# Kernel optimization log

Hardware: AMD Instinct MI355X
Metric: run time of the kernel (lower is better)

The kernel has to match this reference:

```python
import jax, jax.numpy as jnp
import numpy as np

N_NODES = 100000
N_EDGES = 3200000
N_GRAPHS = 256
D = 3
H = 32


def _pointnet_layer(h, pos, src, dst, Wa, ba, Wb, bb):
    # PyG convention: edge_index = [src(j), dst(i)]; message uses h_j, pos_j - pos_i
    edge_feat = jnp.concatenate([h[src], pos[src] - pos[dst]], axis=-1)  # [E, Cin+D]
    msg = jax.nn.relu(edge_feat @ Wa + ba) @ Wb + bb                     # [E, H]
    agg = jax.ops.segment_max(msg, dst, num_segments=N_NODES)           # [N, H]
    # PyG scatter-max fills nodes with no incoming edges with 0
    return jnp.where(jnp.isneginf(agg), 0.0, agg)


def setup_inputs() -> dict:
    key = jax.random.key(0)
    ks = jax.random.split(key, 12)
    pos = jax.random.normal(ks[0], (N_NODES, D), dtype=jnp.float32)
    edge_index = jax.random.randint(ks[1], (2, N_EDGES), 0, N_NODES, dtype=jnp.int32)
    batch = jnp.sort(jax.random.randint(ks[2], (N_NODES,), 0, N_GRAPHS, dtype=jnp.int32))
    def lin(k, fan_in, fan_out):
        bound = 1.0 / np.sqrt(fan_in)
        kw, kb = jax.random.split(k)
        W = jax.random.uniform(kw, (fan_in, fan_out), minval=-bound, maxval=bound, dtype=jnp.float32)
        b = jax.random.uniform(kb, (fan_out,), minval=-bound, maxval=bound, dtype=jnp.float32)
        return W, b
    W1a, b1a = lin(ks[3], D + D, H)
    W1b, b1b = lin(ks[4], H, H)
    W2a, b2a = lin(ks[5], H + D, H)
    W2b, b2b = lin(ks[6], H, H)
    Wout, bout = lin(ks[7], H, 1)
    return {"pos": pos, "edge_index": edge_index, "batch": batch,
            "W1a": W1a, "b1a": b1a, "W1b": W1b, "b1b": b1b,
            "W2a": W2a, "b2a": b2a, "W2b": W2b, "b2b": b2b,
            "Wout": Wout, "bout": bout}


def reference(pos, edge_index, batch, W1a, b1a, W1b, b1b, W2a, b2a, W2b, b2b, Wout, bout):
    src, dst = edge_index[0], edge_index[1]
    h = _pointnet_layer(pos, pos, src, dst, W1a, b1a, W1b, b1b)
    h = jax.nn.relu(h)
    h = _pointnet_layer(h, pos, src, dst, W2a, b2a, W2b, b2b)
    h = jax.nn.relu(h)
    g = jax.ops.segment_max(h, batch, num_segments=N_GRAPHS)  # global_max_pool -> [B, H]
    g = jnp.where(jnp.isneginf(g), 0.0, g)
    return g @ Wout + bout  # [B, 1]
```

## Files before the change

### kernel.cpp

```cpp
#include <hip/hip_runtime.h>

#define NN 100000
#define NE 3200000
#define NG 256
#define H 32
#define SB ((NN + 255) / 256)

typedef __attribute__((ext_vector_type(8))) short b16x8;
typedef __attribute__((ext_vector_type(4))) float f32x4;

union ABfrag { unsigned u[4]; b16x8 v; };

__global__ __launch_bounds__(256) void k_init(unsigned* __restrict__ g,
                                              unsigned* __restrict__ hist) {
    int i = blockIdx.x * 256 + threadIdx.x;
    if (i < NG * H) g[i] = 0u;
    if (i < NN) hist[i] = 0u;
}

__global__ __launch_bounds__(64) void k_packw(const float* __restrict__ W1b,
                                              const float* __restrict__ W2b,
                                              unsigned* __restrict__ Wpk) {
    int l = threadIdx.x;
    int n = l & 15, gq = l >> 4;
    for (int layer = 0; layer < 2; layer++) {
        const float* W = layer ? W2b : W1b;
        for (int h = 0; h < 2; h++) {
            unsigned hi[8], lo[8];
#pragma unroll
            for (int i = 0; i < 8; i++) {
                float w = W[(8 * gq + i) * H + h * 16 + n];
                unsigned wb = __float_as_uint(w);
                unsigned hb = wb & 0xffff0000u;
                float r = w - __uint_as_float(hb);
                hi[i] = hb;
                lo[i] = __float_as_uint(r) & 0xffff0000u;
            }
            unsigned* dh = Wpk + (((layer * 4 + h * 2 + 0) * 64) + l) * 4;
            unsigned* dl = Wpk + (((layer * 4 + h * 2 + 1) * 64) + l) * 4;
#pragma unroll
            for (int w2 = 0; w2 < 4; w2++) {
                dh[w2] = (hi[2 * w2] >> 16) | (hi[2 * w2 + 1] & 0xffff0000u);
                dl[w2] = (lo[2 * w2] >> 16) | (lo[2 * w2 + 1] & 0xffff0000u);
            }
        }
    }
}

__global__ __launch_bounds__(256) void k_hist(const int* __restrict__ dst,
                                              unsigned* __restrict__ hist) {
    int e = blockIdx.x * 256 + threadIdx.x;
    atomicAdd(&hist[dst[e]], 1u);
}

__global__ __launch_bounds__(256) void k_scan1(const unsigned* __restrict__ hist,
                                               unsigned* __restrict__ pre,
                                               unsigned* __restrict__ bsum) {
    __shared__ unsigned sd[256];
    int tid = threadIdx.x;
    int i = blockIdx.x * 256 + tid;
    unsigned v = (i < NN) ? hist[i] : 0u;
    sd[tid] = v;
    __syncthreads();
    for (int off = 1; off < 256; off <<= 1) {
        unsigned t = (tid >= off) ? sd[tid - off] : 0u;
        __syncthreads();
        sd[tid] += t;
        __syncthreads();
    }
    if (i < NN) pre[i] = sd[tid] - v;
    if (tid == 255) bsum[blockIdx.x] = sd[255];
}

__global__ __launch_bounds__(512) void k_scan2(const unsigned* __restrict__ bsum,
                                               unsigned* __restrict__ bpre) {
    __shared__ unsigned sd[512];
    int t = threadIdx.x;
    unsigned v = (t < SB) ? bsum[t] : 0u;
    sd[t] = v;
    __syncthreads();
    for (int off = 1; off < 512; off <<= 1) {
        unsigned x = (t >= off) ? sd[t - off] : 0u;
        __syncthreads();
        sd[t] += x;
        __syncthreads();
    }
    if (t < SB) bpre[t] = sd[t] - v;
}

__global__ __launch_bounds__(256) void k_scan3(const unsigned* __restrict__ pre,
                                               const unsigned* __restrict__ bpre,
                                               const unsigned* __restrict__ hist,
                                               unsigned* __restrict__ cursors,
                                               unsigned* __restrict__ ends) {
    int i = blockIdx.x * 256 + threadIdx.x;
    if (i < NN) {
        unsigned o = pre[i] + bpre[blockIdx.x];
        cursors[i] = o;
        ends[i] = o + hist[i];
    }
}

__global__ __launch_bounds__(256) void k_scatter(const int* __restrict__ src,
                                                 const int* __restrict__ dst,
                                                 unsigned* __restrict__ cursors,
                                                 unsigned* __restrict__ srcS) {
    int e = blockIdx.x * 256 + threadIdx.x;
    int d = dst[e];
    unsigned slot = atomicAdd(&cursors[d], 1u);
    srcS[slot] = (unsigned)src[e];
}

__global__ __launch_bounds__(256) void k_pre1(const float* __restrict__ pos,
                                              const float* __restrict__ W1a,
                                              const float* __restrict__ b1a,
                                              float* __restrict__ E) {
    int n = blockIdx.x * 256 + threadIdx.x;
    if (n >= NN) return;
    float p0 = pos[3 * n], p1 = pos[3 * n + 1], p2 = pos[3 * n + 2];
    float ev[H];
#pragma unroll
    for (int k = 0; k < H; k++) {
        float v = b1a[k];
        v = fmaf(p0, W1a[k] + W1a[96 + k], v);
        v = fmaf(p1, W1a[32 + k] + W1a[128 + k], v);
        v = fmaf(p2, W1a[64 + k] + W1a[160 + k], v);
        ev[k] = v;
    }
    float4* E4 = (float4*)(E + (size_t)n * H);
#pragma unroll
    for (int r = 0; r < 8; r++)
        E4[r] = make_float4(ev[4 * r], ev[4 * r + 1], ev[4 * r + 2], ev[4 * r + 3]);
}

__global__ __launch_bounds__(256) void k_pre2(const float* __restrict__ pos,
                                              const float* __restrict__ agg,
                                              const float* __restrict__ W2a,
                                              const float* __restrict__ b2a,
                                              float* __restrict__ E) {
    int n = blockIdx.x * 256 + threadIdx.x;
    if (n >= NN) return;
    float h[H];
    const float4* A4 = (const float4*)(agg + (size_t)n * H);
#pragma unroll
    for (int r = 0; r < 8; r++) {
        float4 u = A4[r];
        h[4 * r + 0] = u.x; h[4 * r + 1] = u.y;
        h[4 * r + 2] = u.z; h[4 * r + 3] = u.w;
    }
    float p0 = pos[3 * n], p1 = pos[3 * n + 1], p2 = pos[3 * n + 2];
    float ev[H];
#pragma unroll
    for (int k = 0; k < H; k++) {
        float v = b2a[k];
        v = fmaf(p0, W2a[32 * H + k], v);
        v = fmaf(p1, W2a[33 * H + k], v);
        v = fmaf(p2, W2a[34 * H + k], v);
        ev[k] = v;
    }
#pragma unroll
    for (int j = 0; j < H; j++) {
        float hj = h[j];
#pragma unroll
        for (int k = 0; k < H; k++) ev[k] = fmaf(hj, W2a[j * H + k], ev[k]);
    }
    float4* E4 = (float4*)(E + (size_t)n * H);
#pragma unroll
    for (int r = 0; r < 8; r++)
        E4[r] = make_float4(ev[4 * r], ev[4 * r + 1], ev[4 * r + 2], ev[4 * r + 3]);
}

__global__ __launch_bounds__(256) void k_edge(const unsigned* __restrict__ srcS,
                                              const unsigned* __restrict__ ends,
                                              const float* __restrict__ pos,
                                              const float* __restrict__ E,
                                              const float* __restrict__ Wf,
                                              const unsigned* __restrict__ WpkL,
                                              const float* __restrict__ bb,
                                              float* __restrict__ aggOut,
                                              const int* __restrict__ batch,
                                              unsigned* __restrict__ g,
                                              int layer2) {
    int lane = threadIdx.x & 63;
    int node = __builtin_amdgcn_readfirstlane(blockIdx.x * 4 + (threadIdx.x >> 6));
    unsigned start = (node == 0) ? 0u : ends[node - 1];
    int deg = (int)(ends[node] - start);
    int row = lane & 15;
    int j0 = (lane >> 4) << 3;
    ABfrag b0h, b0l, b1h, b1l;
    {
        const uint4* W4 = (const uint4*)WpkL;
        *(uint4*)b0h.u = W4[0 * 64 + lane];
        *(uint4*)b0l.u = W4[1 * 64 + lane];
        *(uint4*)b1h.u = W4[2 * 64 + lane];
        *(uint4*)b1l.u = W4[3 * 64 + lane];
    }
    float pd0 = pos[3 * node], pd1 = pos[3 * node + 1], pd2 = pos[3 * node + 2];
    float fd[8];
#pragma unroll
    for (int q = 0; q < 8; q++)
        fd[q] = fmaf(pd0, Wf[j0 + q],
                fmaf(pd1, Wf[32 + j0 + q], pd2 * Wf[64 + j0 + q]));
    f32x4 vmax0 = {-3.0e38f, -3.0e38f, -3.0e38f, -3.0e38f};
    f32x4 vmax1 = vmax0;
    const f32x4 z = {0.f, 0.f, 0.f, 0.f};
    for (int i0 = 0; i0 < deg; i0 += 16) {
        int e = i0 + row;
        if (e >= deg) e = deg - 1;
        int s = (int)srcS[start + e];
        const float* er = E + ((size_t)s << 5) + j0;
        float4 t0 = *(const float4*)er;
        float4 t1 = *(const float4*)(er + 4);
        float t[8] = {t0.x, t0.y, t0.z, t0.w, t1.x, t1.y, t1.z, t1.w};
        ABfrag ah, al;
#pragma unroll
        for (int w = 0; w < 4; w++) {
            float x0 = fmaxf(t[2 * w]     - fd[2 * w],     0.f);
            float x1 = fmaxf(t[2 * w + 1] - fd[2 * w + 1], 0.f);
            unsigned u0 = __float_as_uint(x0), u1 = __float_as_uint(x1);
            ah.u[w] = __builtin_amdgcn_perm(u1, u0, 0x07060302u);
            float r0 = x0 - __uint_as_float(u0 & 0xffff0000u);
            float r1 = x1 - __uint_as_float(u1 & 0xffff0000u);
            al.u[w] = __builtin_amdgcn_perm(__float_as_uint(r1),
                                            __float_as_uint(r0), 0x07060302u);
        }
        f32x4 acc0 = __builtin_amdgcn_mfma_f32_16x16x32_bf16(ah.v, b0h.v, z, 0, 0, 0);
        acc0 = __builtin_amdgcn_mfma_f32_16x16x32_bf16(al.v, b0h.v, acc0, 0, 0, 0);
        acc0 = __builtin_amdgcn_mfma_f32_16x16x32_bf16(ah.v, b0l.v, acc0, 0, 0, 0);
        f32x4 acc1 = __builtin_amdgcn_mfma_f32_16x16x32_bf16(ah.v, b1h.v, z, 0, 0, 0);
        acc1 = __builtin_amdgcn_mfma_f32_16x16x32_bf16(al.v, b1h.v, acc1, 0, 0, 0);
        acc1 = __builtin_amdgcn_mfma_f32_16x16x32_bf16(ah.v, b1l.v, acc1, 0, 0, 0);
#pragma unroll
        for (int r = 0; r < 4; r++) {
            vmax0[r] = fmaxf(vmax0[r], acc0[r]);
            vmax1[r] = fmaxf(vmax1[r], acc1[r]);
        }
    }
    float m0 = fmaxf(fmaxf(vmax0[0], vmax0[1]), fmaxf(vmax0[2], vmax0[3]));
    float m1 = fmaxf(fmaxf(vmax1[0], vmax1[1]), fmaxf(vmax1[2], vmax1[3]));
    m0 = fmaxf(m0, __shfl_xor(m0, 16));
    m0 = fmaxf(m0, __shfl_xor(m0, 32));
    m1 = fmaxf(m1, __shfl_xor(m1, 16));
    m1 = fmaxf(m1, __shfl_xor(m1, 32));
    if (lane < H) {
        float red = (lane < 16) ? m0 : m1;
        float val = (deg > 0) ? fmaxf(red + bb[lane], 0.f) : 0.f;
        if (!layer2) {
            aggOut[(size_t)node * H + lane] = val;
        } else {
            int b = batch[node];
            unsigned bits = __float_as_uint(val);
            unsigned* gb = g + ((size_t)b << 5) + lane;
            if (bits > *gb) atomicMax(gb, bits);
        }
    }
}

__global__ __launch_bounds__(256) void k_out(const unsigned* __restrict__ g,
                                             const float* __restrict__ Wout,
                                             const float* __restrict__ bout,
                                             float* __restrict__ out) {
    int bidx = threadIdx.x;
    float acc = bout[0];
#pragma unroll
    for (int k = 0; k < H; k++)
        acc = fmaf(__uint_as_float(g[bidx * H + k]), Wout[k], acc);
    out[bidx] = acc;
}

extern "C" void kernel_launch(void* const* d_in, const int* in_sizes, int n_in,
                              void* d_out, int out_size, void* d_ws, size_t ws_size,
                              hipStream_t stream) {
    const float* pos  = (const float*)d_in[0];
    const int* src    = (const int*)d_in[1];
    const int* dst    = src + NE;
    const int* batch  = (const int*)d_in[2];
    const float* W1a  = (const float*)d_in[3];
    const float* b1a  = (const float*)d_in[4];
    const float* W1b  = (const float*)d_in[5];
    const float* b1b  = (const float*)d_in[6];
    const float* W2a  = (const float*)d_in[7];
    const float* b2a  = (const float*)d_in[8];
    const float* W2b  = (const float*)d_in[9];
    const float* b2b  = (const float*)d_in[10];
    const float* Wout = (const float*)d_in[11];
    const float* bout = (const float*)d_in[12];
    float* out = (float*)d_out;

    const size_t SZ = (size_t)NN * H;
    float*    agg  = (float*)d_ws;
    float*    E    = (float*)d_ws + SZ;
    unsigned* srcS = (unsigned*)d_ws + 2 * SZ;
    unsigned* g    = (unsigned*)d_ws + 3 * SZ;
    unsigned* ends = g + NG * H;
    unsigned* bsum = ends + NN;
    unsigned* bpre = bsum + SB + 1;
    unsigned* Wpk  = bpre + SB + 1;
    unsigned* hist    = (unsigned*)agg;
    unsigned* pre     = hist + NN;
    unsigned* cursors = pre + NN;

    const int EDGE_BLOCKS = NE / 256;
    const int NODE_BLOCKS = SB;
    const int WAVE_BLOCKS = NN / 4;

    k_init<<<NODE_BLOCKS, 256, 0, stream>>>(g, hist);
    k_packw<<<1, 64, 0, stream>>>(W1b, W2b, Wpk);
    k_hist<<<EDGE_BLOCKS, 256, 0, stream>>>(dst, hist);
    k_scan1<<<NODE_BLOCKS, 256, 0, stream>>>(hist, pre, bsum);
    k_scan2<<<1, 512, 0, stream>>>(bsum, bpre);
    k_scan3<<<NODE_BLOCKS, 256, 0, stream>>>(pre, bpre, hist, cursors, ends);
    k_scatter<<<EDGE_BLOCKS, 256, 0, stream>>>(src, dst, cursors, srcS);
    k_pre1<<<NODE_BLOCKS, 256, 0, stream>>>(pos, W1a, b1a, E);
    k_edge<<<WAVE_BLOCKS, 256, 0, stream>>>(srcS, ends, pos, E,
                                            W1a + 3 * H, Wpk, b1b,
                                            agg, batch, g, 0);
    k_pre2<<<NODE_BLOCKS, 256, 0, stream>>>(pos, agg, W2a, b2a, E);
    k_edge<<<WAVE_BLOCKS, 256, 0, stream>>>(srcS, ends, pos, E,
                                            W2a + 32 * H, Wpk + 1024, b2b,
                                            agg, batch, g, 1);
    k_out<<<1, 256, 0, stream>>>(g, Wout, bout, out);
}
```

Measured before the change: 758.3 us.

## Two-pass bucketed CSR scatter to localize atomic and write traffic

Replaces the single random scatter of edges into CSR order with a two-pass approach. The first pass partitions edges into 98 coarse destination buckets of 1024 nodes each, using block-local histograms and a packed src/dst-low-bits staging buffer. The second pass does the per-node atomic cursor scatter with bucket-local addresses, which should improve cache locality of atomics and srcS writes. The cost is an extra pass over all edges, a binary search per edge, and reuse of the E buffer as staging.

```diff
diff --git a/kernel.cpp b/kernel.cpp
--- a/kernel.cpp
+++ b/kernel.cpp
@@ -5,6 +5,9 @@
 #define NG 256
 #define H 32
 #define SB ((NN + 255) / 256)
+#define NB 98
+#define BK_SH 10
+#define PART_BLOCKS ((NE + 4095) / 4096)
 
 typedef __attribute__((ext_vector_type(8))) short b16x8;
 typedef __attribute__((ext_vector_type(4))) float f32x4;
@@ -12,10 +15,12 @@
 union ABfrag { unsigned u[4]; b16x8 v; };
 
 __global__ __launch_bounds__(256) void k_init(unsigned* __restrict__ g,
-                                              unsigned* __restrict__ hist) {
+                                              unsigned* __restrict__ hist,
+                                              unsigned* __restrict__ bktcnt) {
     int i = blockIdx.x * 256 + threadIdx.x;
     if (i < NG * H) g[i] = 0u;
     if (i < NN) hist[i] = 0u;
+    if (i < NB) bktcnt[i] = 0u;
 }
 
 __global__ __launch_bounds__(64) void k_packw(const float* __restrict__ W1b,
@@ -48,9 +53,26 @@
 }
 
 __global__ __launch_bounds__(256) void k_hist(const int* __restrict__ dst,
-                                              unsigned* __restrict__ hist) {
-    int e = blockIdx.x * 256 + threadIdx.x;
-    atomicAdd(&hist[dst[e]], 1u);
+                                              unsigned* __restrict__ hist,
+                                              unsigned* __restrict__ bktcnt) {
+    __shared__ unsigned lb[NB];
+    int tid = threadIdx.x;
+    if (tid < NB) lb[tid] = 0u;
+    __syncthreads();
+    int base = blockIdx.x * 4096 + tid;
+    for (int c = 0; c < 16; c++) {
+        int e = base + c * 256;
+        if (e < NE) {
+            int d = dst[e];
+            atomicAdd(&hist[d], 1u);
+            atomicAdd(&lb[d >> BK_SH], 1u);
+        }
+    }
+    __syncthreads();
+    if (tid < NB) {
+        unsigned v = lb[tid];
+        if (v) atomicAdd(&bktcnt[tid], v);
+    }
 }
 
 __global__ __launch_bounds__(256) void k_scan1(const unsigned* __restrict__ hist,
@@ -101,14 +123,67 @@
     }
 }
 
-__global__ __launch_bounds__(256) void k_scatter(const int* __restrict__ src,
-                                                 const int* __restrict__ dst,
-                                                 unsigned* __restrict__ cursors,
-                                                 unsigned* __restrict__ srcS) {
-    int e = blockIdx.x * 256 + threadIdx.x;
-    int d = dst[e];
+__global__ __launch_bounds__(128) void k_bscan(const unsigned* __restrict__ bktcnt,
+                                               unsigned* __restrict__ bktbase,
+                                               unsigned* __restrict__ bktcur) {
+    __shared__ unsigned sd[128];
+    int t = threadIdx.x;
+    unsigned v = (t < NB) ? bktcnt[t] : 0u;
+    sd[t] = v;
+    __syncthreads();
+    for (int off = 1; off < 128; off <<= 1) {
+        unsigned x = (t >= off) ? sd[t - off] : 0u;
+        __syncthreads();
+        sd[t] += x;
+        __syncthreads();
+    }
+    if (t < NB) { bktbase[t] = sd[t] - v; bktcur[t] = sd[t] - v; }
+    if (t == 127) bktbase[NB] = NE;
+}
+
+__global__ __launch_bounds__(256) void k_part(const int* __restrict__ src,
+                                              const int* __restrict__ dst,
+                                              unsigned* __restrict__ bktcur,
+                                              unsigned* __restrict__ staging) {
+    __shared__ unsigned lh[NB], lcur[NB];
+    int tid = threadIdx.x;
+    if (tid < NB) lh[tid] = 0u;
+    __syncthreads();
+    int base = blockIdx.x * 4096 + tid;
+    for (int c = 0; c < 16; c++) {
+        int e = base + c * 256;
+        if (e < NE) atomicAdd(&lh[dst[e] >> BK_SH], 1u);
+    }
+    __syncthreads();
+    if (tid < NB) {
+        unsigned v = lh[tid];
+        lcur[tid] = v ? atomicAdd(&bktcur[tid], v) : 0u;
+    }
+    __syncthreads();
+    for (int c = 0; c < 16; c++) {
+        int e = base + c * 256;
+        if (e < NE) {
+            int d = dst[e], s = src[e];
+            unsigned off = atomicAdd(&lcur[d >> BK_SH], 1u);
+            staging[off] = ((unsigned)s << BK_SH) | (unsigned)(d & ((1 << BK_SH) - 1));
+        }
+    }
+}
+
+__global__ __launch_bounds__(256) void k_scat2(const unsigned* __restrict__ staging,
+                                               const unsigned* __restrict__ bktbase,
+                                               unsigned* __restrict__ cursors,
+                                               unsigned* __restrict__ srcS) {
+    int i = blockIdx.x * 256 + threadIdx.x;
+    unsigned p = staging[i];
+    int lo = 0, hi = NB - 1;
+    while (lo < hi) {
+        int mid = (lo + hi + 1) >> 1;
+        if ((unsigned)i >= bktbase[mid]) lo = mid; else hi = mid - 1;
+    }
+    int d = (lo << BK_SH) | (int)(p & ((1u << BK_SH) - 1));
     unsigned slot = atomicAdd(&cursors[d], 1u);
-    srcS[slot] = (unsigned)src[e];
+    srcS[slot] = p >> BK_SH;
 }
 
 __global__ __launch_bounds__(256) void k_pre1(const float* __restrict__ pos,
@@ -296,21 +371,27 @@
     unsigned* bsum = ends + NN;
     unsigned* bpre = bsum + SB + 1;
     unsigned* Wpk  = bpre + SB + 1;
+    unsigned* bktcnt  = Wpk + 4096;
+    unsigned* bktbase = bktcnt + NB;
+    unsigned* bktcur  = bktbase + NB + 1;
     unsigned* hist    = (unsigned*)agg;
     unsigned* pre     = hist + NN;
     unsigned* cursors = pre + NN;
-
-    const int EDGE_BLOCKS = NE / 256;
+    unsigned* staging = (unsigned*)E;
+
     const int NODE_BLOCKS = SB;
+    const int SCAT_BLOCKS = NE / 256;
     const int WAVE_BLOCKS = NN / 4;
 
-    k_init<<<NODE_BLOCKS, 256, 0, stream>>>(g, hist);
+    k_init<<<NODE_BLOCKS, 256, 0, stream>>>(g, hist, bktcnt);
     k_packw<<<1, 64, 0, stream>>>(W1b, W2b, Wpk);
-    k_hist<<<EDGE_BLOCKS, 256, 0, stream>>>(dst, hist);
+    k_hist<<<PART_BLOCKS, 256, 0, stream>>>(dst, hist, bktcnt);
     k_scan1<<<NODE_BLOCKS, 256, 0, stream>>>(hist, pre, bsum);
     k_scan2<<<1, 512, 0, stream>>>(bsum, bpre);
     k_scan3<<<NODE_BLOCKS, 256, 0, stream>>>(pre, bpre, hist, cursors, ends);
-    k_scatter<<<EDGE_BLOCKS, 256, 0, stream>>>(src, dst, cursors, srcS);
+    k_bscan<<<1, 128, 0, stream>>>(bktcnt, bktbase, bktcur);
+    k_part<<<PART_BLOCKS, 256, 0, stream>>>(src, dst, bktcur, staging);
+    k_scat2<<<SCAT_BLOCKS, 256, 0, stream>>>(staging, bktbase, cursors, srcS);
     k_pre1<<<NODE_BLOCKS, 256, 0, stream>>>(pos, W1a, b1a, E);
     k_edge<<<WAVE_BLOCKS, 256, 0, stream>>>(srcS, ends, pos, E,
                                             W1a + 3 * H, Wpk, b1b,
```

Result: faster. 656.9 us, median of 2 (-13.4%).
